# Optimization experiments

Measured on AMD Instinct MI355X. Metric: run time of the kernel, lower is better.

## Reference

```python
import jax, jax.numpy as jnp
import numpy as np

B, T, I, H, O = 128, 256, 64, 1024, 64


def setup_inputs() -> dict:
    key = jax.random.key(0)
    ks = jax.random.split(key, 16)
    s_ih1 = 1.0 / np.sqrt(H)
    def mk(k, shape, s):
        return jax.random.uniform(k, shape, jnp.float32, -s, s)
    return {
        "x": jax.random.normal(ks[0], (B, T, I), jnp.float32),
        # RNNCell 1: input I -> hidden H
        "W_ih1": mk(ks[1], (H, I), s_ih1),
        "b_ih1": mk(ks[2], (H,), s_ih1),
        "W_hh1": mk(ks[3], (H, H), s_ih1),
        "b_hh1": mk(ks[4], (H,), s_ih1),
        # RNNCell 2: hidden H -> hidden H
        "W_ih2": mk(ks[5], (H, H), s_ih1),
        "b_ih2": mk(ks[6], (H,), s_ih1),
        "W_hh2": mk(ks[7], (H, H), s_ih1),
        "b_hh2": mk(ks[8], (H,), s_ih1),
        # gate: 2H -> H
        "Wg": mk(ks[9], (H, 2 * H), 1.0 / np.sqrt(2 * H)),
        "bg": mk(ks[10], (H,), 1.0 / np.sqrt(2 * H)),
        # output heads: H -> O
        "Wo1": mk(ks[11], (O, H), s_ih1),
        "bo1": mk(ks[12], (O,), s_ih1),
        "Wo2": mk(ks[13], (O, H), s_ih1),
        "bo2": mk(ks[14], (O,), s_ih1),
    }


def reference(x, W_ih1, b_ih1, W_hh1, b_hh1, W_ih2, b_ih2, W_hh2, b_hh2,
              Wg, bg, Wo1, bo1, Wo2, bo2):
    batch = x.shape[0]
    h1_0 = jnp.zeros((batch, H), x.dtype)
    h2_0 = jnp.zeros((batch, H), x.dtype)
    u_0 = jnp.ones((batch, H), x.dtype)

    def step(carry, x_t):
        h1, h2, u = carry
        # RNNCell 1
        h1 = jnp.tanh(x_t @ W_ih1.T + b_ih1 + h1 @ W_hh1.T + b_hh1)
        # RNNCell 2, gated convex blend with previous h2
        h2_new = jnp.tanh(h1 @ W_ih2.T + b_ih2 + h2 @ W_hh2.T + b_hh2)
        h2 = u * h2_new + (1.0 - u) * h2
        # dual tanh output head
        out = jnp.tanh(h1 @ Wo1.T + bo1) + jnp.tanh(h2 @ Wo2.T + bo2)
        # gate for NEXT step, computed from current hiddens
        u = jax.nn.sigmoid(jnp.concatenate([h1, h2], axis=1) @ Wg.T + bg)
        return (h1, h2, u), out

    xs = jnp.swapaxes(x, 0, 1)  # [T, B, I]
    _, outs = jax.lax.scan(step, (h1_0, h2_0, u_0), xs)
    return jnp.swapaxes(outs, 0, 1)  # [B, T, O]
```

## Files before the change

### kernel.cpp

```cpp
#include <hip/hip_runtime.h>
#include <cstddef>

using bf16x8 = __attribute__((ext_vector_type(8))) short;
using f32x4  = __attribute__((ext_vector_type(4))) float;

constexpr int Bb = 128;
constexpr int Tt = 256;
constexpr int Hh = 1024;
constexpr int Oo = 64;
constexpr int NBLK = 200;
constexpr int FLAG_STRIDE = 32;
constexpr int RS = 1048;

constexpr int R_H1 = 8;
constexpr int R_H2 = 16;
constexpr int R_PP = 6;
constexpr int R_PO = 16;

constexpr int FH1 = 0;
constexpr int FP2 = 64;
constexpr int FPG = 96;
constexpr int FPO = 128;
constexpr int FH2 = 160;
constexpr int FZO = 224;

__device__ __forceinline__ float bf2f(short s) {
  unsigned int u = ((unsigned int)(unsigned short)s) << 16;
  float f;
  __builtin_memcpy(&f, &u, 4);
  return f;
}
__device__ __forceinline__ short f2bf(float f) {
  unsigned int u;
  __builtin_memcpy(&u, &f, 4);
  u += 0x7fffu + ((u >> 16) & 1u);
  return (short)(u >> 16);
}
__device__ __forceinline__ bf16x8 as_bf(int4 v) {
  union { int4 i; bf16x8 b; } u; u.i = v; return u.b;
}
__device__ __forceinline__ float ldf(const float* p) {
  return __hip_atomic_load((float*)p, __ATOMIC_RELAXED, __HIP_MEMORY_SCOPE_AGENT);
}
__device__ __forceinline__ void stf(float* p, float v) {
  __hip_atomic_store(p, v, __ATOMIC_RELAXED, __HIP_MEMORY_SCOPE_AGENT);
}
__device__ __forceinline__ unsigned ldu(const unsigned* p) {
  return __hip_atomic_load((unsigned*)p, __ATOMIC_RELAXED, __HIP_MEMORY_SCOPE_AGENT);
}

#define LD16A(d, p) asm volatile("global_load_dwordx4 %0, %1, off sc1" \
                                 : "=v"(d) : "v"((const void*)(p)))

__device__ __forceinline__ void stage_issue(int4 (&r)[16], const short* src, int tid) {
  const int row = tid >> 3;
  const int c0  = (tid & 7) * 8;
  const short* gp = src + (size_t)row * Hh + c0;
#pragma unroll
  for (int j = 0; j < 16; ++j) LD16A(r[j], gp + j * 64);
}
__device__ __forceinline__ void stage_write(short* dstAs, int4 (&r)[16], int tid) {
  const int row = tid >> 3;
  const int c0  = (tid & 7) * 8;
  short* lp = dstAs + row * RS + c0;
  asm volatile("s_waitcnt vmcnt(0)" ::: "memory");
#pragma unroll
  for (int j = 0; j < 16; ++j) *(int4*)(lp + j * 64) = r[j];
}
__device__ __forceinline__ void stage_chunk(short* dstAs, const short* src, int tid) {
  int4 r[16];
  stage_issue(r, src, tid);
  stage_write(dstAs, r, tid);
}

__device__ __forceinline__ void loadW(int4 (&w)[32], const short* B, size_t st,
                                      int lm, int q) {
  const short* bp = B + (size_t)lm * st + q * 8;
#pragma unroll
  for (int c = 0; c < 32; ++c) w[c] = *(const int4*)(bp + c * 32);
}

__device__ __forceinline__ void passW2(const short* As32, int lm, int q,
    const int4 (&w)[32], f32x4& acc0, f32x4& acc1) {
  const short* ap0 = As32 + lm * RS + q * 8;
  const short* ap1 = ap0 + 16 * RS;
#pragma unroll
  for (int c = 0; c < 32; ++c) {
    const bf16x8 a0 = as_bf(*(const int4*)(ap0 + c * 32));
    const bf16x8 a1 = as_bf(*(const int4*)(ap1 + c * 32));
    const bf16x8 b  = as_bf(w[c]);
    acc0 = __builtin_amdgcn_mfma_f32_16x16x32_bf16(a0, b, acc0, 0, 0, 0);
    acc1 = __builtin_amdgcn_mfma_f32_16x16x32_bf16(a1, b, acc1, 0, 0, 0);
  }
}

__device__ __forceinline__ void poll_ge(const unsigned* flags, int base,
                                        int mask, unsigned gen) {
  const unsigned* f = flags + (size_t)(base + (threadIdx.x & mask)) * FLAG_STRIDE;
  while (!__all(ldu(f) >= gen))
    __builtin_amdgcn_s_sleep(2);
}

#define POST_FLAG(SLOT, GEN) do {                                          \
    asm volatile("s_waitcnt vmcnt(0) lgkmcnt(0)" ::: "memory");            \
    __syncthreads();                                                       \
    if (tid == 0)                                                          \
      __hip_atomic_store(p.flags + (size_t)(SLOT) * FLAG_STRIDE,           \
                         (unsigned)(GEN),                                  \
                         __ATOMIC_RELAXED, __HIP_MEMORY_SCOPE_AGENT);      \
  } while (0)

#define ST_BF16_PAIR(BASE, ROW, COL, HV) do {                              \
    const int _ov = __shfl_xor((int)(unsigned short)(HV), 1, 64);          \
    if ((lm & 1) == 0) {                                                   \
      const unsigned _pk = (unsigned)(unsigned short)(HV) | ((unsigned)_ov << 16); \
      __hip_atomic_store((unsigned*)((BASE) + (size_t)(ROW) * Hh + (COL)), _pk, \
                         __ATOMIC_RELAXED, __HIP_MEMORY_SCOPE_AGENT);      \
    } } while (0)

struct RP {
  short *h1ring;
  short *h2ring;
  float *h2f;
  float *pre2f;
  float *pg1f;
  float *po1f;
  const short* prex;
  const short *whh1, *wih2, *whh2, *wg, *wo1, *wo2;
  const float *b_ih2, *b_hh2, *bg, *bo1, *bo2;
  float* out;
  unsigned* flags;
};

__global__ void __launch_bounds__(256, 1) rnn_kernel(RP p) {
  __shared__ short As[64 * RS];
  __shared__ float zbuf[2048];
  const int tid = threadIdx.x;
  const int lane = tid & 63;
  const int wv = tid >> 6;
  const int lm = lane & 15;
  const int q = lane >> 4;
  const int bid = blockIdx.x;

  const size_t HS = (size_t)Bb * Hh;
  const f32x4 z4 = {0.f, 0.f, 0.f, 0.f};
  int4 w[32];

  if (bid < 64) {
    const int g = bid;
    const int rg = g >> 4;
    const int mb = rg * 32, cb = (g & 15) * 64;
    const int cw = cb + wv * 16;
    loadW(w, p.whh1 + (size_t)cw * Hh, Hh, lm, q);
    for (int t = 0; t < Tt; ++t) {
      short prs[2][4];
      const short* pr = p.prex + (size_t)t * HS;
#pragma unroll
      for (int rf = 0; rf < 2; ++rf)
#pragma unroll
        for (int r = 0; r < 4; ++r)
          prs[rf][r] = pr[(size_t)(mb + rf * 16 + q * 4 + r) * Hh + cw + lm];
      if (tid < 64 && t >= 1) poll_ge(p.flags, FH1 + rg * 16, 15, (unsigned)t);
      __syncthreads();
      const short* h1prev = p.h1ring + (size_t)((t + R_H1 - 1) % R_H1) * HS;
      stage_chunk(As, h1prev + (size_t)mb * Hh, tid);
      __syncthreads();
      f32x4 a0 = z4, a1 = z4;
      passW2(As, lm, q, w, a0, a1);
      if (tid < 64 && t >= 8) {
        poll_ge(p.flags, FP2 + (rg >> 1) * 16, 15, (unsigned)(t - 7));
        poll_ge(p.flags, FPG + (rg >> 1) * 16, 15, (unsigned)(t - 7));
        poll_ge(p.flags, FPO + rg, 0, (unsigned)(t - 7));
      }
      __syncthreads();
      short* h1out = p.h1ring + (size_t)(t % R_H1) * HS;
#pragma unroll
      for (int rf = 0; rf < 2; ++rf)
#pragma unroll
        for (int r = 0; r < 4; ++r) {
          const int row = mb + rf * 16 + q * 4 + r;
          const float z = rf ? a1[r] : a0[r];
          const short hv = f2bf(tanhf(z + bf2f(prs[rf][r])));
          ST_BF16_PAIR(h1out, row, cw + lm, hv);
        }
      POST_FLAG(FH1 + g, t + 1);
    }
  } else if (bid < 128) {
    const bool isP2 = (bid < 96);
    const int g = isP2 ? (bid - 64) : (bid - 96);
    const int rgp = g >> 4, cg = g & 15;
    const int mb = rgp * 64, cb = cg * 64;
    const int cw = cb + wv * 16;
    float bias;
    if (isP2) {
      bias = p.b_ih2[cw + lm] + p.b_hh2[cw + lm];
      loadW(w, p.wih2 + (size_t)cw * Hh, Hh, lm, q);
    } else {
      bias = p.bg[cw + lm];
      loadW(w, p.wg + (size_t)cw * (2 * Hh), 2 * Hh, lm, q);
    }
    const int fslot = (isP2 ? FP2 : FPG) + g;
    const int gslot = FH2 + rgp * 32 + cg * 2;
    const int glag = isP2 ? 5 : 4;
    for (int t = 0; t < Tt; ++t) {
      if (tid < 64) poll_ge(p.flags, FH1 + rgp * 32, 31, (unsigned)(t + 1));
      __syncthreads();
      const short* h1cur = p.h1ring + (size_t)(t % R_H1) * HS;
      stage_chunk(As, h1cur + (size_t)mb * Hh, tid);
      __syncthreads();
      int4 rB[16];
      stage_issue(rB, h1cur + (size_t)(mb + 32) * Hh, tid);
      f32x4 acc[4];
      acc[0] = acc[1] = acc[2] = acc[3] = (f32x4){bias, bias, bias, bias};
      passW2(As, lm, q, w, acc[0], acc[1]);
      stage_write(As + 32 * RS, rB, tid);
      __syncthreads();
      passW2(As + 32 * RS, lm, q, w, acc[2], acc[3]);
      if (tid < 64 && t >= R_PP) poll_ge(p.flags, gslot, 1, (unsigned)(t - glag));
      __syncthreads();
      float* dst = (isP2 ? p.pre2f : p.pg1f) + (size_t)(t % R_PP) * HS;
#pragma unroll
      for (int rf = 0; rf < 4; ++rf)
#pragma unroll
        for (int r = 0; r < 4; ++r) {
          const int row = mb + rf * 16 + q * 4 + r;
          stf(dst + (size_t)row * Hh + cw + lm, acc[rf][r]);
        }
      POST_FLAG(fslot, t + 1);
    }
  } else if (bid < 192) {
    const int g = bid - 128;
    const int rgh = g >> 5, cb = (g & 31) * 32;
    const int mb = rgh * 64;
    const int m = wv >> 1;
    const int ch = wv & 1;
    const int cw = cb + ch * 16;
    const int fp2slot = FP2 + rgh * 16 + (cb >> 6);
    const int fpgslot = FPG + rgh * 16 + (cb >> 6);
    if (m == 0) loadW(w, p.whh2 + (size_t)cw * Hh, Hh, lm, q);
    else        loadW(w, p.wg + Hh + (size_t)cw * (2 * Hh), 2 * Hh, lm, q);
    for (int s = 0; s < Tt; ++s) {
      if (tid < 64) {
        poll_ge(p.flags, fp2slot, 0, (unsigned)(s + 1));
        if (s >= 1) {
          poll_ge(p.flags, fpgslot, 0, (unsigned)s);
          poll_ge(p.flags, FH2 + rgh * 32, 31, (unsigned)s);
        }
      }
      __syncthreads();
      const short* h2prev = p.h2ring + (size_t)((s + R_H2 - 1) % R_H2) * HS;
      stage_chunk(As, h2prev + (size_t)mb * Hh, tid);
      __syncthreads();
      int4 rB[16];
      stage_issue(rB, h2prev + (size_t)(mb + 32) * Hh, tid);
      f32x4 acc[4];
      acc[0] = acc[1] = acc[2] = acc[3] = z4;
      passW2(As, lm, q, w, acc[0], acc[1]);
      stage_write(As + 32 * RS, rB, tid);
      __syncthreads();
      float p2v[4][4], pg1v[4][4], hpv[4][4];
      if (m == 0) {
        const float* pre2s = p.pre2f + (size_t)(s % R_PP) * HS;
        const float* pg1s  = p.pg1f + (size_t)((s + R_PP - 1) % R_PP) * HS;
#pragma unroll
        for (int rf = 0; rf < 4; ++rf)
#pragma unroll
          for (int r = 0; r < 4; ++r) {
            const size_t idx = (size_t)(mb + rf * 16 + q * 4 + r) * Hh + cw + lm;
            p2v[rf][r] = ldf(pre2s + idx);
            pg1v[rf][r] = (s > 0) ? ldf(pg1s + idx) : 0.f;
            hpv[rf][r] = p.h2f[idx];
          }
      }
      passW2(As + 32 * RS, lm, q, w, acc[2], acc[3]);
      if (m == 1) {
        float* zb = zbuf + ch * 1024;
#pragma unroll
        for (int rf = 0; rf < 4; ++rf)
#pragma unroll
          for (int r = 0; r < 4; ++r)
            zb[(rf * 4 + r) * 64 + lane] = acc[rf][r];
      }
      if (tid < 64 && s >= R_H2) poll_ge(p.flags, FZO + rgh * 2, 1, (unsigned)(s - 15));
      __syncthreads();
      if (m == 0) {
        const float* zb = zbuf + ch * 1024;
        short* h2out = p.h2ring + (size_t)(s % R_H2) * HS;
#pragma unroll
        for (int rf = 0; rf < 4; ++rf)
#pragma unroll
          for (int r = 0; r < 4; ++r) {
            const int row = mb + rf * 16 + q * 4 + r;
            const size_t idx = (size_t)row * Hh + cw + lm;
            const float zg = zb[(rf * 4 + r) * 64 + lane];
            const float u = (s == 0) ? 1.f
                : 1.f / (1.f + expf(-(zg + pg1v[rf][r])));
            const float hn = tanhf(acc[rf][r] + p2v[rf][r]);
            const float nv = fmaf(u, hn - hpv[rf][r], hpv[rf][r]);
            p.h2f[idx] = nv;
            const short hv = f2bf(nv);
            ST_BF16_PAIR(h2out, row, cw + lm, hv);
          }
      }
      POST_FLAG(FH2 + g, s + 1);
    }
  } else if (bid < 196) {
    const int g = bid - 192;
    const int mb = g * 32;
    const int cw = wv * 16;
    const float bias = p.bo1[cw + lm];
    loadW(w, p.wo1 + (size_t)cw * Hh, Hh, lm, q);
    for (int t = 0; t < Tt; ++t) {
      if (tid < 64) poll_ge(p.flags, FH1 + g * 16, 15, (unsigned)(t + 1));
      __syncthreads();
      const short* h1cur = p.h1ring + (size_t)(t % R_H1) * HS;
      stage_chunk(As, h1cur + (size_t)mb * Hh, tid);
      __syncthreads();
      f32x4 a0 = {bias, bias, bias, bias}, a1 = a0;
      passW2(As, lm, q, w, a0, a1);
      if (tid < 64 && t >= R_PO) poll_ge(p.flags, FZO + g, 0, (unsigned)(t - 15));
      __syncthreads();
      float* dst = p.po1f + (size_t)(t % R_PO) * (Bb * Oo);
#pragma unroll
      for (int rf = 0; rf < 2; ++rf)
#pragma unroll
        for (int r = 0; r < 4; ++r) {
          const int row = mb + rf * 16 + q * 4 + r;
          const float z = rf ? a1[r] : a0[r];
          stf(dst + (size_t)row * Oo + cw + lm, tanhf(z));
        }
      POST_FLAG(FPO + g, t + 1);
    }
  } else {
    const int g = bid - 196;
    const int mb = g * 32;
    const int cw = wv * 16;
    const float bias = p.bo2[cw + lm];
    loadW(w, p.wo2 + (size_t)cw * Hh, Hh, lm, q);
    for (int ot = 0; ot < Tt; ++ot) {
      if (tid < 64) {
        poll_ge(p.flags, FH2 + (g >> 1) * 32, 31, (unsigned)(ot + 1));
        poll_ge(p.flags, FPO + g, 0, (unsigned)(ot + 1));
      }
      __syncthreads();
      float pv[2][4];
      const float* po1s = p.po1f + (size_t)(ot % R_PO) * (Bb * Oo);
#pragma unroll
      for (int rf = 0; rf < 2; ++rf)
#pragma unroll
        for (int r = 0; r < 4; ++r)
          pv[rf][r] = ldf(po1s + (size_t)(mb + rf * 16 + q * 4 + r) * Oo + cw + lm);
      const short* h2cur = p.h2ring + (size_t)(ot % R_H2) * HS;
      stage_chunk(As, h2cur + (size_t)mb * Hh, tid);
      __syncthreads();
      f32x4 a0 = {bias, bias, bias, bias}, a1 = a0;
      passW2(As, lm, q, w, a0, a1);
#pragma unroll
      for (int rf = 0; rf < 2; ++rf)
#pragma unroll
        for (int r = 0; r < 4; ++r) {
          const int row = mb + rf * 16 + q * 4 + r;
          const float z = rf ? a1[r] : a0[r];
          p.out[(size_t)row * (Tt * Oo) + (size_t)ot * Oo + cw + lm] =
              pv[rf][r] + tanhf(z);
        }
      POST_FLAG(FZO + g, ot + 1);
    }
  }
}

__global__ void __launch_bounds__(256) prex_kernel(
    const float* __restrict__ x, const float* __restrict__ wih1,
    const float* __restrict__ b_ih1, const float* __restrict__ b_hh1,
    short* __restrict__ prex) {
  const int tid = threadIdx.x;
  const int lane = tid & 63;
  const int wv = tid >> 6;
  const int lm = lane & 15;
  const int q = lane >> 4;
  const int bm = blockIdx.x >> 4;
  const int bn = blockIdx.x & 15;
  const int rowbase = bm * 64;
  const int col = bn * 64 + wv * 16 + lm;

  const f32x4 z4 = {0.f, 0.f, 0.f, 0.f};
  f32x4 acc[4];
#pragma unroll
  for (int mt = 0; mt < 4; ++mt) acc[mt] = z4;

#pragma unroll
  for (int kc = 0; kc < 2; ++kc) {
    const float* bp = wih1 + col * 64 + kc * 32 + q * 8;
    bf16x8 bf;
#pragma unroll
    for (int j = 0; j < 8; ++j) bf[j] = f2bf(bp[j]);
#pragma unroll
    for (int mt = 0; mt < 4; ++mt) {
      const float* ap = x + (size_t)(rowbase + mt * 16 + lm) * 64 + kc * 32 + q * 8;
      bf16x8 af;
#pragma unroll
      for (int j = 0; j < 8; ++j) af[j] = f2bf(ap[j]);
      acc[mt] = __builtin_amdgcn_mfma_f32_16x16x32_bf16(af, bf, acc[mt], 0, 0, 0);
    }
  }
  const float bia = b_ih1[col] + b_hh1[col];
#pragma unroll
  for (int mt = 0; mt < 4; ++mt) {
#pragma unroll
    for (int r = 0; r < 4; ++r) {
      const int row = rowbase + mt * 16 + q * 4 + r;
      const int b  = row >> 8;
      const int tt = row & 255;
      prex[((size_t)tt * Bb + b) * Hh + col] = f2bf(acc[mt][r] + bia);
    }
  }
}

__global__ void conv_kernel(const float* __restrict__ s, short* __restrict__ d, int n) {
  int i = blockIdx.x * blockDim.x + threadIdx.x;
  const int stride = gridDim.x * blockDim.x;
  for (; i < n; i += stride) d[i] = f2bf(s[i]);
}

__global__ void init_kernel(short* h1ring, short* h2ring,
                            float* h2f, unsigned* flags) {
  const int i = blockIdx.x * blockDim.x + threadIdx.x;
  const size_t HS = (size_t)Bb * Hh;
  h1ring[(size_t)(R_H1 - 1) * HS + i] = 0;
  h2ring[(size_t)(R_H2 - 1) * HS + i] = 0;
  h2f[i] = 0.f;
  if (i < 256) flags[i * FLAG_STRIDE] = 0u;
}

extern "C" void kernel_launch(void* const* d_in, const int* in_sizes, int n_in,
                              void* d_out, int out_size, void* d_ws, size_t ws_size,
                              hipStream_t stream) {
  (void)in_sizes; (void)n_in; (void)out_size; (void)ws_size;
  const float* x      = (const float*)d_in[0];
  const float* W_ih1  = (const float*)d_in[1];
  const float* b_ih1  = (const float*)d_in[2];
  const float* W_hh1  = (const float*)d_in[3];
  const float* b_hh1  = (const float*)d_in[4];
  const float* W_ih2  = (const float*)d_in[5];
  const float* b_ih2  = (const float*)d_in[6];
  const float* W_hh2  = (const float*)d_in[7];
  const float* b_hh2  = (const float*)d_in[8];
  const float* Wg     = (const float*)d_in[9];
  const float* bg     = (const float*)d_in[10];
  const float* Wo1    = (const float*)d_in[11];
  const float* bo1    = (const float*)d_in[12];
  const float* Wo2    = (const float*)d_in[13];
  const float* bo2    = (const float*)d_in[14];

  char* ws = (char*)d_ws;
  size_t off = 0;
  auto alloc = [&](size_t bytes) -> void* {
    void* ptr = ws + off;
    off += (bytes + 255) & ~(size_t)255;
    return ptr;
  };
  short* whh1 = (short*)alloc((size_t)Hh * Hh * 2);
  short* wih2 = (short*)alloc((size_t)Hh * Hh * 2);
  short* whh2 = (short*)alloc((size_t)Hh * Hh * 2);
  short* wg   = (short*)alloc((size_t)Hh * 2 * Hh * 2);
  short* wo1  = (short*)alloc((size_t)Oo * Hh * 2);
  short* wo2  = (short*)alloc((size_t)Oo * Hh * 2);
  short* prex = (short*)alloc((size_t)Bb * Tt * Hh * 2);
  short* h1ring = (short*)alloc((size_t)R_H1 * Bb * Hh * 2);
  short* h2ring = (short*)alloc((size_t)R_H2 * Bb * Hh * 2);
  float* h2f  = (float*)alloc((size_t)Bb * Hh * 4);
  float* pre2f= (float*)alloc((size_t)R_PP * Bb * Hh * 4);
  float* pg1f = (float*)alloc((size_t)R_PP * Bb * Hh * 4);
  float* po1f = (float*)alloc((size_t)R_PO * Bb * Oo * 4);
  unsigned* flags = (unsigned*)alloc(256 * FLAG_STRIDE * 4);

  conv_kernel<<<1024, 256, 0, stream>>>(W_hh1, whh1, Hh * Hh);
  conv_kernel<<<1024, 256, 0, stream>>>(W_ih2, wih2, Hh * Hh);
  conv_kernel<<<1024, 256, 0, stream>>>(W_hh2, whh2, Hh * Hh);
  conv_kernel<<<2048, 256, 0, stream>>>(Wg,    wg,   Hh * 2 * Hh);
  conv_kernel<<<256,  256, 0, stream>>>(Wo1,   wo1,  Oo * Hh);
  conv_kernel<<<256,  256, 0, stream>>>(Wo2,   wo2,  Oo * Hh);
  init_kernel<<<512, 256, 0, stream>>>(h1ring, h2ring, h2f, flags);
  prex_kernel<<<8192, 256, 0, stream>>>(x, W_ih1, b_ih1, b_hh1, prex);

  RP p;
  p.h1ring = h1ring; p.h2ring = h2ring;
  p.h2f = h2f; p.pre2f = pre2f; p.pg1f = pg1f; p.po1f = po1f;
  p.prex = prex;
  p.whh1 = whh1; p.wih2 = wih2; p.whh2 = whh2;
  p.wg = wg; p.wo1 = wo1; p.wo2 = wo2;
  p.b_ih2 = b_ih2; p.b_hh2 = b_hh2;
  p.bg = bg; p.bo1 = bo1; p.bo2 = bo2;
  p.out = (float*)d_out;
  p.flags = flags;

  rnn_kernel<<<NBLK, 256, 0, stream>>>(p);
}
```

Measured before the change: 2.743 ms.

## Halve persistent block count by doubling threads per block to 512

Reorganises the persistent pipelined RNN kernel from 200 blocks of 256 threads to 100 blocks of 512 threads. Each role (h1, pre2/gate, h2, output heads) now covers twice the columns or rows per block, and the flag slots and poll counts are remapped to match. This halves the number of inter-block flag waits per step and the amount of redundant staging of the shared h-slice into LDS. The cost is more waves per CU contending for LDS, and the output-head blocks leave half their waves idle.

```diff
diff --git a/kernel.cpp b/kernel.cpp
--- a/kernel.cpp
+++ b/kernel.cpp
@@ -8,7 +8,7 @@
 constexpr int Tt = 256;
 constexpr int Hh = 1024;
 constexpr int Oo = 64;
-constexpr int NBLK = 200;
+constexpr int NBLK = 100;
 constexpr int FLAG_STRIDE = 32;
 constexpr int RS = 1048;
 
@@ -18,11 +18,11 @@
 constexpr int R_PO = 16;
 
 constexpr int FH1 = 0;
-constexpr int FP2 = 64;
-constexpr int FPG = 96;
-constexpr int FPO = 128;
-constexpr int FH2 = 160;
-constexpr int FZO = 224;
+constexpr int FP2 = 32;
+constexpr int FPG = 48;
+constexpr int FH2 = 64;
+constexpr int FPO = 96;
+constexpr int FZO = 98;
 
 __device__ __forceinline__ float bf2f(short s) {
   unsigned int u = ((unsigned int)(unsigned short)s) << 16;
@@ -52,23 +52,23 @@
 #define LD16A(d, p) asm volatile("global_load_dwordx4 %0, %1, off sc1" \
                                  : "=v"(d) : "v"((const void*)(p)))
 
-__device__ __forceinline__ void stage_issue(int4 (&r)[16], const short* src, int tid) {
-  const int row = tid >> 3;
-  const int c0  = (tid & 7) * 8;
+__device__ __forceinline__ void stage_issue(int4 (&r)[8], const short* src, int tid) {
+  const int row = tid >> 4;
+  const int c0  = (tid & 15) * 8;
   const short* gp = src + (size_t)row * Hh + c0;
 #pragma unroll
-  for (int j = 0; j < 16; ++j) LD16A(r[j], gp + j * 64);
-}
-__device__ __forceinline__ void stage_write(short* dstAs, int4 (&r)[16], int tid) {
-  const int row = tid >> 3;
-  const int c0  = (tid & 7) * 8;
+  for (int j = 0; j < 8; ++j) LD16A(r[j], gp + j * 128);
+}
+__device__ __forceinline__ void stage_write(short* dstAs, int4 (&r)[8], int tid) {
+  const int row = tid >> 4;
+  const int c0  = (tid & 15) * 8;
   short* lp = dstAs + row * RS + c0;
   asm volatile("s_waitcnt vmcnt(0)" ::: "memory");
 #pragma unroll
-  for (int j = 0; j < 16; ++j) *(int4*)(lp + j * 64) = r[j];
+  for (int j = 0; j < 8; ++j) *(int4*)(lp + j * 128) = r[j];
 }
 __device__ __forceinline__ void stage_chunk(short* dstAs, const short* src, int tid) {
-  int4 r[16];
+  int4 r[8];
   stage_issue(r, src, tid);
   stage_write(dstAs, r, tid);
 }
@@ -132,9 +132,9 @@
   unsigned* flags;
 };
 
-__global__ void __launch_bounds__(256, 1) rnn_kernel(RP p) {
+__global__ void __launch_bounds__(512, 1) rnn_kernel(RP p) {
   __shared__ short As[64 * RS];
-  __shared__ float zbuf[2048];
+  __shared__ float zbuf[4096];
   const int tid = threadIdx.x;
   const int lane = tid & 63;
   const int wv = tid >> 6;
@@ -146,10 +146,9 @@
   const f32x4 z4 = {0.f, 0.f, 0.f, 0.f};
   int4 w[32];
 
-  if (bid < 64) {
-    const int g = bid;
-    const int rg = g >> 4;
-    const int mb = rg * 32, cb = (g & 15) * 64;
+  if (bid < 32) {
+    const int rg = bid >> 3, cg = bid & 7;
+    const int mb = rg * 32, cb = cg * 128;
     const int cw = cb + wv * 16;
     loadW(w, p.whh1 + (size_t)cw * Hh, Hh, lm, q);
     for (int t = 0; t < Tt; ++t) {
@@ -160,7 +159,7 @@
 #pragma unroll
         for (int r = 0; r < 4; ++r)
           prs[rf][r] = pr[(size_t)(mb + rf * 16 + q * 4 + r) * Hh + cw + lm];
-      if (tid < 64 && t >= 1) poll_ge(p.flags, FH1 + rg * 16, 15, (unsigned)t);
+      if (tid < 64 && t >= 1) poll_ge(p.flags, FH1 + rg * 8, 7, (unsigned)t);
       __syncthreads();
       const short* h1prev = p.h1ring + (size_t)((t + R_H1 - 1) % R_H1) * HS;
       stage_chunk(As, h1prev + (size_t)mb * Hh, tid);
@@ -168,9 +167,9 @@
       f32x4 a0 = z4, a1 = z4;
       passW2(As, lm, q, w, a0, a1);
       if (tid < 64 && t >= 8) {
-        poll_ge(p.flags, FP2 + (rg >> 1) * 16, 15, (unsigned)(t - 7));
-        poll_ge(p.flags, FPG + (rg >> 1) * 16, 15, (unsigned)(t - 7));
-        poll_ge(p.flags, FPO + rg, 0, (unsigned)(t - 7));
+        poll_ge(p.flags, FP2 + (rg >> 1) * 8, 7, (unsigned)(t - 7));
+        poll_ge(p.flags, FPG + (rg >> 1) * 8, 7, (unsigned)(t - 7));
+        poll_ge(p.flags, FPO + (rg >> 1), 0, (unsigned)(t - 7));
       }
       __syncthreads();
       short* h1out = p.h1ring + (size_t)(t % R_H1) * HS;
@@ -183,13 +182,13 @@
           const short hv = f2bf(tanhf(z + bf2f(prs[rf][r])));
           ST_BF16_PAIR(h1out, row, cw + lm, hv);
         }
-      POST_FLAG(FH1 + g, t + 1);
-    }
-  } else if (bid < 128) {
-    const bool isP2 = (bid < 96);
-    const int g = isP2 ? (bid - 64) : (bid - 96);
-    const int rgp = g >> 4, cg = g & 15;
-    const int mb = rgp * 64, cb = cg * 64;
+      POST_FLAG(FH1 + bid, t + 1);
+    }
+  } else if (bid < 64) {
+    const bool isP2 = (bid < 48);
+    const int g = bid - (isP2 ? 32 : 48);
+    const int rgp = g >> 3, cg = g & 7;
+    const int mb = rgp * 64, cb = cg * 128;
     const int cw = cb + wv * 16;
     float bias;
     if (isP2) {
@@ -200,15 +199,15 @@
       loadW(w, p.wg + (size_t)cw * (2 * Hh), 2 * Hh, lm, q);
     }
     const int fslot = (isP2 ? FP2 : FPG) + g;
-    const int gslot = FH2 + rgp * 32 + cg * 2;
+    const int gslot = FH2 + rgp * 16 + cg * 2;
     const int glag = isP2 ? 5 : 4;
     for (int t = 0; t < Tt; ++t) {
-      if (tid < 64) poll_ge(p.flags, FH1 + rgp * 32, 31, (unsigned)(t + 1));
+      if (tid < 64) poll_ge(p.flags, FH1 + rgp * 16, 15, (unsigned)(t + 1));
       __syncthreads();
       const short* h1cur = p.h1ring + (size_t)(t % R_H1) * HS;
       stage_chunk(As, h1cur + (size_t)mb * Hh, tid);
       __syncthreads();
-      int4 rB[16];
+      int4 rB[8];
       stage_issue(rB, h1cur + (size_t)(mb + 32) * Hh, tid);
       f32x4 acc[4];
       acc[0] = acc[1] = acc[2] = acc[3] = (f32x4){bias, bias, bias, bias};
@@ -228,15 +227,15 @@
         }
       POST_FLAG(fslot, t + 1);
     }
-  } else if (bid < 192) {
-    const int g = bid - 128;
-    const int rgh = g >> 5, cb = (g & 31) * 32;
-    const int mb = rgh * 64;
-    const int m = wv >> 1;
-    const int ch = wv & 1;
+  } else if (bid < 96) {
+    const int g = bid - 64;
+    const int rgh = g >> 4, cgh = g & 15;
+    const int mb = rgh * 64, cb = cgh * 64;
+    const int m = wv >> 2;
+    const int ch = wv & 3;
     const int cw = cb + ch * 16;
-    const int fp2slot = FP2 + rgh * 16 + (cb >> 6);
-    const int fpgslot = FPG + rgh * 16 + (cb >> 6);
+    const int fp2slot = FP2 + rgh * 8 + (cgh >> 1);
+    const int fpgslot = FPG + rgh * 8 + (cgh >> 1);
     if (m == 0) loadW(w, p.whh2 + (size_t)cw * Hh, Hh, lm, q);
     else        loadW(w, p.wg + Hh + (size_t)cw * (2 * Hh), 2 * Hh, lm, q);
     for (int s = 0; s < Tt; ++s) {
@@ -244,14 +243,14 @@
         poll_ge(p.flags, fp2slot, 0, (unsigned)(s + 1));
         if (s >= 1) {
           poll_ge(p.flags, fpgslot, 0, (unsigned)s);
-          poll_ge(p.flags, FH2 + rgh * 32, 31, (unsigned)s);
+          poll_ge(p.flags, FH2 + rgh * 16, 15, (unsigned)s);
         }
       }
       __syncthreads();
       const short* h2prev = p.h2ring + (size_t)((s + R_H2 - 1) % R_H2) * HS;
       stage_chunk(As, h2prev + (size_t)mb * Hh, tid);
       __syncthreads();
-      int4 rB[16];
+      int4 rB[8];
       stage_issue(rB, h2prev + (size_t)(mb + 32) * Hh, tid);
       f32x4 acc[4];
       acc[0] = acc[1] = acc[2] = acc[3] = z4;
@@ -281,7 +280,7 @@
           for (int r = 0; r < 4; ++r)
             zb[(rf * 4 + r) * 64 + lane] = acc[rf][r];
       }
-      if (tid < 64 && s >= R_H2) poll_ge(p.flags, FZO + rgh * 2, 1, (unsigned)(s - 15));
+      if (tid < 64 && s >= R_H2) poll_ge(p.flags, FZO + rgh, 0, (unsigned)(s - 15));
       __syncthreads();
       if (m == 0) {
         const float* zb = zbuf + ch * 1024;
@@ -304,10 +303,11 @@
       }
       POST_FLAG(FH2 + g, s + 1);
     }
-  } else if (bid < 196) {
-    const int g = bid - 192;
-    const int mb = g * 32;
-    const int cw = wv * 16;
+  } else if (bid < 98) {
+    const int g = bid - 96;
+    const int mb = g * 64;
+    const int cw = (wv & 3) * 16;
+    const bool act = (wv < 4);
     const float bias = p.bo1[cw + lm];
     loadW(w, p.wo1 + (size_t)cw * Hh, Hh, lm, q);
     for (int t = 0; t < Tt; ++t) {
@@ -316,54 +316,71 @@
       const short* h1cur = p.h1ring + (size_t)(t % R_H1) * HS;
       stage_chunk(As, h1cur + (size_t)mb * Hh, tid);
       __syncthreads();
-      f32x4 a0 = {bias, bias, bias, bias}, a1 = a0;
-      passW2(As, lm, q, w, a0, a1);
+      int4 rB[8];
+      stage_issue(rB, h1cur + (size_t)(mb + 32) * Hh, tid);
+      f32x4 acc[4];
+      acc[0] = acc[1] = acc[2] = acc[3] = (f32x4){bias, bias, bias, bias};
+      if (act) passW2(As, lm, q, w, acc[0], acc[1]);
+      stage_write(As + 32 * RS, rB, tid);
+      __syncthreads();
+      if (act) passW2(As + 32 * RS, lm, q, w, acc[2], acc[3]);
       if (tid < 64 && t >= R_PO) poll_ge(p.flags, FZO + g, 0, (unsigned)(t - 15));
       __syncthreads();
-      float* dst = p.po1f + (size_t)(t % R_PO) * (Bb * Oo);
-#pragma unroll
-      for (int rf = 0; rf < 2; ++rf)
-#pragma unroll
-        for (int r = 0; r < 4; ++r) {
-          const int row = mb + rf * 16 + q * 4 + r;
-          const float z = rf ? a1[r] : a0[r];
-          stf(dst + (size_t)row * Oo + cw + lm, tanhf(z));
-        }
+      if (act) {
+        float* dst = p.po1f + (size_t)(t % R_PO) * (Bb * Oo);
+#pragma unroll
+        for (int rf = 0; rf < 4; ++rf)
+#pragma unroll
+          for (int r = 0; r < 4; ++r) {
+            const int row = mb + rf * 16 + q * 4 + r;
+            stf(dst + (size_t)row * Oo + cw + lm, tanhf(acc[rf][r]));
+          }
+      }
       POST_FLAG(FPO + g, t + 1);
     }
   } else {
-    const int g = bid - 196;
-    const int mb = g * 32;
-    const int cw = wv * 16;
+    const int g = bid - 98;
+    const int mb = g * 64;
+    const int cw = (wv & 3) * 16;
+    const bool act = (wv < 4);
     const float bias = p.bo2[cw + lm];
     loadW(w, p.wo2 + (size_t)cw * Hh, Hh, lm, q);
     for (int ot = 0; ot < Tt; ++ot) {
       if (tid < 64) {
-        poll_ge(p.flags, FH2 + (g >> 1) * 32, 31, (unsigned)(ot + 1));
+        poll_ge(p.flags, FH2 + g * 16, 15, (unsigned)(ot + 1));
         poll_ge(p.flags, FPO + g, 0, (unsigned)(ot + 1));
       }
       __syncthreads();
-      float pv[2][4];
-      const float* po1s = p.po1f + (size_t)(ot % R_PO) * (Bb * Oo);
-#pragma unroll
-      for (int rf = 0; rf < 2; ++rf)
-#pragma unroll
-        for (int r = 0; r < 4; ++r)
-          pv[rf][r] = ldf(po1s + (size_t)(mb + rf * 16 + q * 4 + r) * Oo + cw + lm);
+      float pv[4][4];
+      if (act) {
+        const float* po1s = p.po1f + (size_t)(ot % R_PO) * (Bb * Oo);
+#pragma unroll
+        for (int rf = 0; rf < 4; ++rf)
+#pragma unroll
+          for (int r = 0; r < 4; ++r)
+            pv[rf][r] = ldf(po1s + (size_t)(mb + rf * 16 + q * 4 + r) * Oo + cw + lm);
+      }
       const short* h2cur = p.h2ring + (size_t)(ot % R_H2) * HS;
       stage_chunk(As, h2cur + (size_t)mb * Hh, tid);
       __syncthreads();
-      f32x4 a0 = {bias, bias, bias, bias}, a1 = a0;
-      passW2(As, lm, q, w, a0, a1);
-#pragma unroll
-      for (int rf = 0; rf < 2; ++rf)
-#pragma unroll
-        for (int r = 0; r < 4; ++r) {
-          const int row = mb + rf * 16 + q * 4 + r;
-          const float z = rf ? a1[r] : a0[r];
-          p.out[(size_t)row * (Tt * Oo) + (size_t)ot * Oo + cw + lm] =
-              pv[rf][r] + tanhf(z);
-        }
+      int4 rB[8];
+      stage_issue(rB, h2cur + (size_t)(mb + 32) * Hh, tid);
+      f32x4 acc[4];
+      acc[0] = acc[1] = acc[2] = acc[3] = (f32x4){bias, bias, bias, bias};
+      if (act) passW2(As, lm, q, w, acc[0], acc[1]);
+      stage_write(As + 32 * RS, rB, tid);
+      __syncthreads();
+      if (act) {
+        passW2(As + 32 * RS, lm, q, w, acc[2], acc[3]);
+#pragma unroll
+        for (int rf = 0; rf < 4; ++rf)
+#pragma unroll
+          for (int r = 0; r < 4; ++r) {
+            const int row = mb + rf * 16 + q * 4 + r;
+            p.out[(size_t)row * (Tt * Oo) + (size_t)ot * Oo + cw + lm] =
+                pv[rf][r] + tanhf(acc[rf][r]);
+          }
+      }
       POST_FLAG(FZO + g, ot + 1);
     }
   }
@@ -494,5 +511,5 @@
   p.out = (float*)d_out;
   p.flags = flags;
 
-  rnn_kernel<<<NBLK, 256, 0, stream>>>(p);
-}
+  rnn_kernel<<<NBLK, 512, 0, stream>>>(p);
+}
```

Result: slower. 5.407 ms (+97.2%).
